# Optimization experiments

Measured on AMD Instinct MI355X. Metric: run time of the kernel, lower is better.

The kernel has to match this reference:

```python
import jax, jax.numpy as jnp
import numpy as np

B, S, D, H = 4, 8192, 512, 8
HD = D // H  # head_dim = 64


def setup_inputs() -> dict:
    key0 = jax.random.key(0)
    ks = jax.random.split(key0, 8)
    scale_in = (2.0 / (D + 3 * D)) ** 0.5  # xavier_uniform-ish std
    scale_out = (2.0 / (D + D)) ** 0.5
    return {
        "query": jax.random.normal(ks[0], (B, S, D), dtype=jnp.float32),
        "key": jax.random.normal(ks[1], (B, S, D), dtype=jnp.float32),
        "value": jax.random.normal(ks[2], (B, S, D), dtype=jnp.float32),
        "key_padding_mask": jax.random.bernoulli(ks[3], 0.1, (B, S)),  # True = ignore
        "in_proj_weight": jax.random.normal(ks[4], (3 * D, D), dtype=jnp.float32) * scale_in,
        "in_proj_bias": jnp.zeros((3 * D,), dtype=jnp.float32),
        "out_proj_weight": jax.random.normal(ks[5], (D, D), dtype=jnp.float32) * scale_out,
        "out_proj_bias": jnp.zeros((D,), dtype=jnp.float32),
    }


def _phi(x):
    # ELU+1 feature map (strictly positive)
    return jax.nn.elu(x) + 1.0


def reference(query, key, value, key_padding_mask, in_proj_weight, in_proj_bias,
              out_proj_weight, out_proj_bias):
    # NB: the torch module projects q,k,v all from `query`; key/value args are unused.
    qkv = query @ in_proj_weight.T + in_proj_bias  # (B,S,3D)
    q, k, v = jnp.split(qkv, 3, axis=-1)
    # (B,S,D) -> (B,H,S,HD)
    def to_heads(x):
        return x.reshape(B, S, H, HD).transpose(0, 2, 1, 3)
    q = _phi(to_heads(q))
    k = _phi(to_heads(k))
    v = to_heads(v)
    mask = (~key_padding_mask).astype(q.dtype)[:, None, :, None]  # (B,1,S,1)
    k = k * mask
    v = v * mask
    kv = jnp.einsum('bhsd,bhse->bhde', k, v)          # (B,H,HD,HD)
    numerator = jnp.einsum('bhsd,bhde->bhse', q, kv)  # (B,H,S,HD)
    k_sum = k.sum(axis=2)                              # (B,H,HD)
    denominator = jnp.einsum('bhsd,bhd->bhs', q, k_sum)[..., None]
    denominator = jnp.maximum(denominator, 1e-6)
    attn_out = (numerator / denominator).transpose(0, 2, 1, 3).reshape(B, S, D)
    return attn_out @ out_proj_weight.T + out_proj_bias
```

## Files before the change

### kernel.cpp

```cpp
#include <hip/hip_runtime.h>
#include <cstddef>

#define B_   4
#define S_   8192
#define D_   512
#define H_   8
#define HD_  64
#define NROW (B_ * S_)
#define NQ   ((size_t)NROW * D_)

typedef __attribute__((ext_vector_type(4))) float  f32x4;
typedef __attribute__((ext_vector_type(8))) short  s16x8;
typedef __attribute__((ext_vector_type(4))) unsigned short u16x4;
typedef __attribute__((ext_vector_type(8))) unsigned short u16x8;

__device__ __forceinline__ float phi_f(float x) {
    return x > 0.0f ? x + 1.0f : expf(x);
}
__device__ __forceinline__ float bf2f(unsigned short u) {
    return __uint_as_float(((unsigned int)u) << 16);
}
__device__ __forceinline__ unsigned short f2bf(float f) {
    unsigned int u = __float_as_uint(f);
    u += 0x7fffu + ((u >> 16) & 1u);
    return (unsigned short)(u >> 16);
}

#define GLOBAL_AS(p) ((const __attribute__((address_space(1))) void*)(p))
#define LDS_AS(p)    ((__attribute__((address_space(3))) void*)(p))

__global__ void detect_mask(const unsigned char* __restrict__ m, int* __restrict__ flag) {
    __shared__ int sany;
    if (threadIdx.x == 0) sany = 0;
    __syncthreads();
    const uint4* mw = (const uint4*)m;
    unsigned int any = 0;
    #pragma unroll
    for (int r = 0; r < 8; ++r) {
        const uint4 w = mw[r * 256 + threadIdx.x];
        any |= (w.x | w.y | w.z | w.w) & 0xFFFFFF00u;
    }
    if (any) atomicOr(&sany, 1);
    __syncthreads();
    if (threadIdx.x == 0) *flag = sany ? 1 : 0;
}

__global__ __launch_bounds__(256) void convert_all(
    const float* __restrict__ q,  unsigned short* __restrict__ qb,
    const float* __restrict__ wi, unsigned short* __restrict__ wib,
    const float* __restrict__ wo, unsigned short* __restrict__ wob,
    const unsigned char* __restrict__ kpm, const int* __restrict__ flag,
    float* __restrict__ fmask)
{
    const size_t i = (size_t)blockIdx.x * 256 + threadIdx.x;
    {
        const float4 v = *(const float4*)&q[i * 4];
        u16x4 o; o.x = f2bf(v.x); o.y = f2bf(v.y); o.z = f2bf(v.z); o.w = f2bf(v.w);
        *(u16x4*)&qb[i * 4] = o;
    }
    if (i < 786432 / 4) {
        const float4 v = *(const float4*)&wi[i * 4];
        u16x4 o; o.x = f2bf(v.x); o.y = f2bf(v.y); o.z = f2bf(v.z); o.w = f2bf(v.w);
        *(u16x4*)&wib[i * 4] = o;
    }
    if (i < 262144 / 4) {
        const float4 v = *(const float4*)&wo[i * 4];
        u16x4 o; o.x = f2bf(v.x); o.y = f2bf(v.y); o.z = f2bf(v.z); o.w = f2bf(v.w);
        *(u16x4*)&wob[i * 4] = o;
    }
    if (i < NROW) {
        const bool ignore = (*flag) ? (kpm[i] != 0) : (((const int*)kpm)[i] != 0);
        fmask[i] = ignore ? 0.0f : 1.0f;
    }
}

__global__ __launch_bounds__(256) void gemm_mfma(
    const unsigned short* __restrict__ A,  int lda,
    const unsigned short* __restrict__ Bw, int ldb,
    const float* __restrict__ bias, int K, int mode,
    const float* __restrict__ fmask,
    unsigned short* __restrict__ Cq,
    unsigned short* __restrict__ Ck,
    unsigned short* __restrict__ Cv,
    float* __restrict__ Cout)
{
    __shared__ __align__(16) unsigned short As[3][128 * 32];
    __shared__ __align__(16) unsigned short Bs[3][128 * 32];
    __shared__ float fm[128];

    const int t    = threadIdx.x;
    const int lane = t & 63;
    const int wave = t >> 6;
    const int wm   = wave & 1;
    const int wn   = wave >> 1;

    const int nbx = gridDim.x;
    const int nwg = nbx * gridDim.y;
    int id = blockIdx.y * nbx + blockIdx.x;
    id = (id & 7) * (nwg >> 3) + (id >> 3);
    const int m0 = (id / nbx) * 128;
    const int n0 = (id % nbx) * 128;

    if (mode == 0 && t < 128) fm[t] = fmask[m0 + t];

    f32x4 acc[4][4] = {};

    const int sr  = lane >> 2;
    const int skc = (((lane & 3) ^ ((lane >> 3) & 3))) * 8;

    const int nt = K >> 5;

    #define STAGE(kt_, buf_)                                                            \
        do {                                                                            \
            const int k0_ = (kt_) << 5;                                                 \
            _Pragma("unroll")                                                           \
            for (int j = 0; j < 2; ++j) {                                               \
                const int row = wave * 32 + j * 16;                                     \
                const unsigned short* g = A + (size_t)(m0 + row + sr) * lda + k0_ + skc;\
                __builtin_amdgcn_global_load_lds(GLOBAL_AS(g),                          \
                    LDS_AS(&As[(buf_)][row * 32]), 16, 0, 0);                           \
            }                                                                           \
            _Pragma("unroll")                                                           \
            for (int j = 0; j < 2; ++j) {                                               \
                const int row = wave * 32 + j * 16;                                     \
                const unsigned short* g = Bw + (size_t)(n0 + row + sr) * ldb + k0_ + skc;\
                __builtin_amdgcn_global_load_lds(GLOBAL_AS(g),                          \
                    LDS_AS(&Bs[(buf_)][row * 32]), 16, 0, 0);                           \
            }                                                                           \
        } while (0)

    STAGE(0, 0);
    STAGE(1, 1);

    const int fr = lane & 15;
    const int cn = lane >> 4;
    const int fo = (cn ^ ((fr >> 1) & 3)) * 8;

    int cur = 0;
    for (int kt = 0; kt < nt; ++kt) {
        if (kt + 1 < nt) asm volatile("s_waitcnt vmcnt(4)" ::: "memory");
        else             asm volatile("s_waitcnt vmcnt(0)" ::: "memory");
        __builtin_amdgcn_s_barrier();

        if (kt + 2 < nt) {
            int nb = cur + 2; if (nb >= 3) nb -= 3;
            STAGE(kt + 2, nb);
        }

        s16x8 af[4], bf[4];
        #pragma unroll
        for (int i = 0; i < 4; ++i)
            af[i] = *(const s16x8*)&As[cur][(wm * 64 + i * 16 + fr) * 32 + fo];
        #pragma unroll
        for (int j = 0; j < 4; ++j)
            bf[j] = *(const s16x8*)&Bs[cur][(wn * 64 + j * 16 + fr) * 32 + fo];
        #pragma unroll
        for (int i = 0; i < 4; ++i)
            #pragma unroll
            for (int j = 0; j < 4; ++j)
                acc[i][j] = __builtin_amdgcn_mfma_f32_16x16x32_bf16(af[i], bf[j], acc[i][j], 0, 0, 0);

        if (++cur == 3) cur = 0;
    }
    #undef STAGE

    const int col  = lane & 15;
    const int rowq = (lane >> 4) * 4;
    float bj[4];
    #pragma unroll
    for (int j = 0; j < 4; ++j) bj[j] = bias[n0 + wn * 64 + j * 16 + col];

    if (mode == 1) {
        #pragma unroll
        for (int i = 0; i < 4; ++i)
            #pragma unroll
            for (int r = 0; r < 4; ++r) {
                const int m = m0 + wm * 64 + i * 16 + rowq + r;
                #pragma unroll
                for (int j = 0; j < 4; ++j) {
                    const int n = n0 + wn * 64 + j * 16 + col;
                    Cout[(size_t)m * D_ + n] = acc[i][j][r] + bj[j];
                }
            }
    } else {
        const int region = n0 >> 9;
        unsigned short* Cb = region == 0 ? Cq : (region == 1 ? Ck : Cv);
        #pragma unroll
        for (int i = 0; i < 4; ++i)
            #pragma unroll
            for (int r = 0; r < 4; ++r) {
                const int ml = wm * 64 + i * 16 + rowq + r;
                const int m  = m0 + ml;
                const float mk = fm[ml];
                #pragma unroll
                for (int j = 0; j < 4; ++j) {
                    const int n  = (n0 & 511) + wn * 64 + j * 16 + col;
                    float v = acc[i][j][r] + bj[j];
                    if (region == 0)      v = phi_f(v);
                    else if (region == 1) v = phi_f(v) * mk;
                    else                  v = v * mk;
                    Cb[(size_t)m * D_ + n] = f2bf(v);
                }
            }
    }
}

__global__ __launch_bounds__(256) void kv_reduce(
    const unsigned short* __restrict__ kbuf,
    const unsigned short* __restrict__ vbuf,
    float* __restrict__ part_kv,
    float* __restrict__ part_ks)
{
    const int bh = blockIdx.x, chunk = blockIdx.y;
    const int b = bh >> 3, h = bh & 7;

    __shared__ __align__(16) float Ks[16][68];
    __shared__ __align__(16) float Vs[16][68];

    const int t    = threadIdx.x;
    const int wave = t >> 6;
    const int lane = t & 63;
    const int tx   = lane & 7;
    const int ty   = lane >> 3;

    const int sr = (t & 127) >> 3;
    const int sc = (t & 7) * 8;
    const unsigned short* src = (t < 128 ? kbuf : vbuf) + (size_t)b * S_ * D_ + h * HD_;
    float (*dst)[68] = (t < 128) ? Ks : Vs;

    float acc[8][8] = {};
    float ks[8] = {};
    const int s0 = chunk * (S_ / 16);
    const int NIT = 32;

    u16x8 x = *(const u16x8*)&src[(size_t)(s0 + sr) * D_ + sc];

    for (int it = 0; it < NIT; ++it) {
        __syncthreads();
        float4 f0, f1;
        f0.x = bf2f(x[0]); f0.y = bf2f(x[1]); f0.z = bf2f(x[2]); f0.w = bf2f(x[3]);
        f1.x = bf2f(x[4]); f1.y = bf2f(x[5]); f1.z = bf2f(x[6]); f1.w = bf2f(x[7]);
        *(float4*)&dst[sr][sc]     = f0;
        *(float4*)&dst[sr][sc + 4] = f1;
        __syncthreads();
        u16x8 xn = {};
        if (it + 1 < NIT)
            xn = *(const u16x8*)&src[(size_t)(s0 + (it + 1) * 16 + sr) * D_ + sc];
        #pragma unroll
        for (int ss0 = 0; ss0 < 4; ++ss0) {
            const int ss = wave + ss0 * 4;
            const float4 a0 = *(const float4*)&Ks[ss][ty * 8];
            const float4 a1 = *(const float4*)&Ks[ss][ty * 8 + 4];
            const float4 v0 = *(const float4*)&Vs[ss][tx * 8];
            const float4 v1 = *(const float4*)&Vs[ss][tx * 8 + 4];
            const float av[8] = {a0.x, a0.y, a0.z, a0.w, a1.x, a1.y, a1.z, a1.w};
            const float vv[8] = {v0.x, v0.y, v0.z, v0.w, v1.x, v1.y, v1.z, v1.w};
            #pragma unroll
            for (int i2 = 0; i2 < 8; ++i2)
                #pragma unroll
                for (int j2 = 0; j2 < 8; ++j2)
                    acc[i2][j2] += av[i2] * vv[j2];
            if (tx == 0) {
                #pragma unroll
                for (int i2 = 0; i2 < 8; ++i2) ks[i2] += av[i2];
            }
        }
        x = xn;
    }

    const int p = bh * 64 + chunk * 4 + wave;
    float* pk = part_kv + (size_t)p * 4096;
    #pragma unroll
    for (int i2 = 0; i2 < 8; ++i2) {
        #pragma unroll
        for (int j4 = 0; j4 < 2; ++j4) {
            float4 o;
            o.x = acc[i2][j4 * 4 + 0]; o.y = acc[i2][j4 * 4 + 1];
            o.z = acc[i2][j4 * 4 + 2]; o.w = acc[i2][j4 * 4 + 3];
            *(float4*)&pk[(ty * 8 + i2) * 64 + tx * 8 + j4 * 4] = o;
        }
    }
    if (tx == 0) {
        float* ps = part_ks + (size_t)p * 64;
        #pragma unroll
        for (int i2 = 0; i2 < 8; ++i2) ps[ty * 8 + i2] = ks[i2];
    }
}

__global__ void kv_reduce2(const float* __restrict__ part_kv,
                           const float* __restrict__ part_ks,
                           unsigned short* __restrict__ kvT,
                           unsigned short* __restrict__ ksumb)
{
    const int i = blockIdx.x * 256 + threadIdx.x;
    if (i < 32 * 4096) {
        const int bh = i >> 12, de = i & 4095;
        const int d = de >> 6, e = de & 63;
        float s = 0.0f;
        #pragma unroll
        for (int c = 0; c < 64; ++c) s += part_kv[(size_t)(bh * 64 + c) * 4096 + de];
        kvT[bh * 4096 + e * 64 + d] = f2bf(s);
    }
    if (i < 32 * 64) {
        const int bh = i >> 6, e = i & 63;
        float s = 0.0f;
        #pragma unroll
        for (int c = 0; c < 64; ++c) s += part_ks[(size_t)(bh * 64 + c) * 64 + e];
        ksumb[i] = f2bf(s);
    }
}

__global__ __launch_bounds__(512) void attn_outproj(
    const unsigned short* __restrict__ qphi,
    const unsigned short* __restrict__ kvT,
    const unsigned short* __restrict__ ksumb,
    const unsigned short* __restrict__ wo,
    const float* __restrict__ bias,
    float* __restrict__ out)
{
    __shared__ __align__(16) unsigned short An[64][520];
    __shared__ __align__(16) unsigned short Bs[2][512 * 32];

    const int t    = threadIdx.x;
    const int lane = t & 63;
    const int wv   = t >> 6;
    const int r0   = blockIdx.x * 64;
    const int b    = r0 >> 13;
    const int bh   = b * 8 + wv;

    const int fr = lane & 15;
    const int fk = (lane >> 4) * 8;
    const int rq = (lane >> 4) * 4;

    {
        const unsigned short* Ah = qphi + (size_t)r0 * D_ + wv * HD_;
        const unsigned short* Bh = kvT + bh * 4096;
        const unsigned short* Kh = ksumb + bh * 64;

        s16x8 af[2][4], bfr[2][4], bd[2];
        #pragma unroll
        for (int kc = 0; kc < 2; ++kc) {
            #pragma unroll
            for (int i = 0; i < 4; ++i)
                af[kc][i] = *(const s16x8*)&Ah[(size_t)(i * 16 + fr) * D_ + kc * 32 + fk];
            #pragma unroll
            for (int j = 0; j < 4; ++j)
                bfr[kc][j] = *(const s16x8*)&Bh[(j * 16 + fr) * 64 + kc * 32 + fk];
            bd[kc] = *(const s16x8*)&Kh[kc * 32 + fk];
        }

        f32x4 acc[4][4] = {};
        f32x4 accd[4] = {};
        #pragma unroll
        for (int kc = 0; kc < 2; ++kc)
            #pragma unroll
            for (int i = 0; i < 4; ++i) {
                #pragma unroll
                for (int j = 0; j < 4; ++j)
                    acc[i][j] = __builtin_amdgcn_mfma_f32_16x16x32_bf16(af[kc][i], bfr[kc][j], acc[i][j], 0, 0, 0);
                accd[i] = __builtin_amdgcn_mfma_f32_16x16x32_bf16(af[kc][i], bd[kc], accd[i], 0, 0, 0);
            }

        #pragma unroll
        for (int i = 0; i < 4; ++i)
            #pragma unroll
            for (int r = 0; r < 4; ++r) {
                const float inv = 1.0f / fmaxf(accd[i][r], 1e-6f);
                const int row = i * 16 + rq + r;
                #pragma unroll
                for (int j = 0; j < 4; ++j)
                    An[row][wv * 64 + j * 16 + fr] = f2bf(acc[i][j][r] * inv);
            }
    }

    const int sr  = lane >> 2;
    const int skc = (((lane & 3) ^ ((lane >> 3) & 3))) * 8;
    const int cn  = lane >> 4;
    const int fo  = (cn ^ ((fr >> 1) & 3)) * 8;

    #define WSTAGE(kt_, buf_)                                                           \
        do {                                                                            \
            _Pragma("unroll")                                                           \
            for (int j = 0; j < 4; ++j) {              \
                const int row = wv * 64 + j * 16;                                       \
                const unsigned short* g = wo + (size_t)(row + sr) * D_ + ((kt_) << 5) + skc;\
                __builtin_amdgcn_global_load_lds(GLOBAL_AS(g),                          \
                    LDS_AS(&Bs[(buf_)][row * 32]), 16, 0, 0);                           \
            }                                                                           \
        } while (0)

    WSTAGE(0, 0);
    __syncthreads();

    const int wm2 = wv >> 2;
    const int wn4 = wv & 3;
    f32x4 acc2[2][8] = {};

    for (int kt = 0; kt < 16; ++kt) {
        const int cur = kt & 1;
        if (kt + 1 < 16) WSTAGE(kt + 1, cur ^ 1);

        s16x8 a2[2], b2[8];
        #pragma unroll
        for (int i = 0; i < 2; ++i)
            a2[i] = *(const s16x8*)&An[wm2 * 32 + i * 16 + fr][kt * 32 + fk];
        #pragma unroll
        for (int j = 0; j < 8; ++j)
            b2[j] = *(const s16x8*)&Bs[cur][(wn4 * 128 + j * 16 + fr) * 32 + fo];
        #pragma unroll
        for (int i = 0; i < 2; ++i)
            #pragma unroll
            for (int j = 0; j < 8; ++j)
                acc2[i][j] = __builtin_amdgcn_mfma_f32_16x16x32_bf16(a2[i], b2[j], acc2[i][j], 0, 0, 0);

        __syncthreads();
    }
    #undef WSTAGE

    float bj[8];
    #pragma unroll
    for (int j = 0; j < 8; ++j) bj[j] = bias[wn4 * 128 + j * 16 + fr];

    #pragma unroll
    for (int i = 0; i < 2; ++i)
        #pragma unroll
        for (int r = 0; r < 4; ++r) {
            const int m = r0 + wm2 * 32 + i * 16 + rq + r;
            #pragma unroll
            for (int j = 0; j < 8; ++j)
                out[(size_t)m * D_ + wn4 * 128 + j * 16 + fr] = acc2[i][j][r] + bj[j];
        }
}

extern "C" void kernel_launch(void* const* d_in, const int* in_sizes, int n_in,
                              void* d_out, int out_size, void* d_ws, size_t ws_size,
                              hipStream_t stream)
{
    const float* query       = (const float*)d_in[0];
    const unsigned char* kpm = (const unsigned char*)d_in[3];
    const float* w_in        = (const float*)d_in[4];
    const float* b_in        = (const float*)d_in[5];
    const float* w_out       = (const float*)d_in[6];
    const float* b_out       = (const float*)d_in[7];
    float* out = (float*)d_out;

    unsigned short* qb    = (unsigned short*)d_ws;
    unsigned short* qphi  = qb    + NQ;
    unsigned short* kpb   = qphi  + NQ;
    unsigned short* vmb   = kpb   + NQ;
    unsigned short* wib   = vmb   + NQ;
    unsigned short* wob   = wib   + 1536 * 512;
    float* fmask   = (float*)(wob + 512 * 512);
    float* part_kv = fmask + NROW;
    float* part_ks = part_kv + (size_t)2048 * 4096;
    unsigned short* kvTb  = (unsigned short*)(part_ks + 2048 * 64);
    unsigned short* ksumb = kvTb + 32 * 4096;
    int*   flag    = (int*)(ksumb + 32 * 64);

    hipLaunchKernelGGL(detect_mask, dim3(1), dim3(256), 0, stream, kpm, flag);
    hipLaunchKernelGGL(convert_all, dim3(16384), dim3(256), 0, stream,
                       query, qb, w_in, wib, w_out, wob, kpm, flag, fmask);

    hipLaunchKernelGGL(gemm_mfma, dim3(1536 / 128, NROW / 128), dim3(256), 0, stream,
                       qb, D_, wib, D_, b_in, D_, 0, fmask,
                       qphi, kpb, vmb, (float*)nullptr);

    hipLaunchKernelGGL(kv_reduce, dim3(32, 16), dim3(256), 0, stream, kpb, vmb, part_kv, part_ks);
    hipLaunchKernelGGL(kv_reduce2, dim3(512), dim3(256), 0, stream,
                       part_kv, part_ks, kvTb, ksumb);

    hipLaunchKernelGGL(attn_outproj, dim3(NROW / 64), dim3(512), 0, stream,
                       qphi, kvTb, ksumb, wob, b_out, out);
}
```

Before: 387.6 us.

## Load GEMM B operand directly from global memory and double-buffer only A

```diff
diff --git a/kernel.cpp b/kernel.cpp
--- a/kernel.cpp
+++ b/kernel.cpp
@@ -84,8 +84,7 @@
     unsigned short* __restrict__ Cv,
     float* __restrict__ Cout)
 {
-    __shared__ __align__(16) unsigned short As[3][128 * 32];
-    __shared__ __align__(16) unsigned short Bs[3][128 * 32];
+    __shared__ __align__(16) unsigned short As[2][128 * 32];
     __shared__ float fm[128];
 
     const int t    = threadIdx.x;
@@ -110,42 +109,30 @@
 
     const int nt = K >> 5;
 
-    #define STAGE(kt_, buf_)                                                            \
+    #define STAGE_A(kt_, buf_)                                                          \
         do {                                                                            \
             const int k0_ = (kt_) << 5;                                                 \
             _Pragma("unroll")                                                           \
-            for (int j = 0; j < 2; ++j) {                                               \
+            for (int j = 0; j < 2; ++j) {          \
                 const int row = wave * 32 + j * 16;                                     \
                 const unsigned short* g = A + (size_t)(m0 + row + sr) * lda + k0_ + skc;\
                 __builtin_amdgcn_global_load_lds(GLOBAL_AS(g),                          \
                     LDS_AS(&As[(buf_)][row * 32]), 16, 0, 0);                           \
             }                                                                           \
-            _Pragma("unroll")                                                           \
-            for (int j = 0; j < 2; ++j) {                                               \
-                const int row = wave * 32 + j * 16;                                     \
-                const unsigned short* g = Bw + (size_t)(n0 + row + sr) * ldb + k0_ + skc;\
-                __builtin_amdgcn_global_load_lds(GLOBAL_AS(g),                          \
-                    LDS_AS(&Bs[(buf_)][row * 32]), 16, 0, 0);                           \
-            }                                                                           \
         } while (0)
 
-    STAGE(0, 0);
-    STAGE(1, 1);
+    STAGE_A(0, 0);
+    __syncthreads();
 
     const int fr = lane & 15;
     const int cn = lane >> 4;
     const int fo = (cn ^ ((fr >> 1) & 3)) * 8;
 
-    int cur = 0;
+    const unsigned short* Bbase = Bw + (size_t)(n0 + wn * 64 + fr) * ldb + cn * 8;
+
     for (int kt = 0; kt < nt; ++kt) {
-        if (kt + 1 < nt) asm volatile("s_waitcnt vmcnt(4)" ::: "memory");
-        else             asm volatile("s_waitcnt vmcnt(0)" ::: "memory");
-        __builtin_amdgcn_s_barrier();
-
-        if (kt + 2 < nt) {
-            int nb = cur + 2; if (nb >= 3) nb -= 3;
-            STAGE(kt + 2, nb);
-        }
+        const int cur = kt & 1;
+        if (kt + 1 < nt) STAGE_A(kt + 1, cur ^ 1);
 
         s16x8 af[4], bf[4];
         #pragma unroll
@@ -153,16 +140,16 @@
             af[i] = *(const s16x8*)&As[cur][(wm * 64 + i * 16 + fr) * 32 + fo];
         #pragma unroll
         for (int j = 0; j < 4; ++j)
-            bf[j] = *(const s16x8*)&Bs[cur][(wn * 64 + j * 16 + fr) * 32 + fo];
+            bf[j] = *(const s16x8*)&Bbase[(size_t)(j * 16) * ldb + kt * 32];
         #pragma unroll
         for (int i = 0; i < 4; ++i)
             #pragma unroll
             for (int j = 0; j < 4; ++j)
                 acc[i][j] = __builtin_amdgcn_mfma_f32_16x16x32_bf16(af[i], bf[j], acc[i][j], 0, 0, 0);
 
-        if (++cur == 3) cur = 0;
-    }
-    #undef STAGE
+        __syncthreads();
+    }
+    #undef STAGE_A
 
     const int col  = lane & 15;
     const int rowq = (lane >> 4) * 4;
```

New measurement: 426.9 us. 10.1% more time.
